# Performance work log

Measured on AMD Instinct MI355X. Metric: run time of the kernel, lower is better.

Reference implementation:

```python
import jax, jax.numpy as jnp
import numpy as np
from jax import lax

D_MODEL = 1024
D_STATE = 128
D_CONV = 4
EXPAND = 2
N_HEADS = 32
CHUNK = 64
D_INNER = EXPAND * D_MODEL                 # 2048
CONV_DIM = D_INNER + 2 * D_STATE           # 2304
D_IN_PROJ = 2 * D_INNER + 2 * D_STATE + N_HEADS  # 4384
HEAD_DIM = D_INNER // N_HEADS              # 64
EPS = 1e-5


def setup_inputs() -> dict:
    key = jax.random.key(0)
    ks = jax.random.split(key, 10)
    u = jax.random.normal(ks[0], (4, 4096, D_MODEL), dtype=jnp.float32)
    in_proj_w = jax.random.normal(ks[1], (D_IN_PROJ, D_MODEL), dtype=jnp.float32) * 0.02
    conv_w = jax.random.normal(ks[2], (CONV_DIM, 1, D_CONV), dtype=jnp.float32) * 0.3
    conv_b = jnp.zeros((CONV_DIM,), dtype=jnp.float32)
    dt_bias = jax.random.uniform(ks[3], (N_HEADS,), minval=-0.5, maxval=0.5, dtype=jnp.float32)
    A_log = jax.random.uniform(ks[4], (N_HEADS,), minval=-0.1, maxval=-0.01, dtype=jnp.float32)
    D = jax.random.uniform(ks[5], (N_HEADS,), minval=0.9, maxval=1.1, dtype=jnp.float32)
    norm_w = jnp.ones((D_INNER,), dtype=jnp.float32)
    out_proj_w = jax.random.normal(ks[6], (D_MODEL, D_INNER), dtype=jnp.float32) * 0.02
    return {"u": u, "in_proj_w": in_proj_w, "conv_w": conv_w, "conv_b": conv_b,
            "dt_bias": dt_bias, "A_log": A_log, "D": D, "norm_w": norm_w,
            "out_proj_w": out_proj_w}


def segsum(x):
    """Stable segment sum. x: (..., T) -> (..., T, T); exp of it is 1-semiseparable."""
    T = x.shape[-1]
    xe = jnp.broadcast_to(x[..., :, None], x.shape + (T,))  # '... d -> ... d e'
    mask_strict = jnp.tril(jnp.ones((T, T), dtype=bool), k=-1)
    xe = jnp.where(mask_strict, xe, 0.0)
    seg = jnp.cumsum(xe, axis=-2)
    mask_incl = jnp.tril(jnp.ones((T, T), dtype=bool), k=0)
    return jnp.where(mask_incl, seg, -jnp.inf)


def ssd(x, A, B, C):
    """x:(b,L,h,p)  A:(b,L,h)  B,C:(b,L,h,n). L multiple of CHUNK."""
    b, Lp, h, p = x.shape
    n = B.shape[-1]
    c = Lp // CHUNK
    x = x.reshape(b, c, CHUNK, h, p)
    A = A.reshape(b, c, CHUNK, h).transpose(0, 3, 1, 2)       # (b,h,c,l)
    B = B.reshape(b, c, CHUNK, h, n)
    C = C.reshape(b, c, CHUNK, h, n)
    A_cumsum = jnp.cumsum(A, axis=-1)                          # (b,h,c,l)
    L = jnp.exp(segsum(A))                                     # (b,h,c,l,l)
    # intra-chunk (diagonal blocks)
    Y_diag = jnp.einsum('bclhn,bcshn,bhcls,bcshp->bclhp', C, B, L, x)
    # chunk-final states
    decay_states = jnp.exp(A_cumsum[:, :, :, -1:] - A_cumsum)  # (b,h,c,l)
    states = jnp.einsum('bclhn,bhcl,bclhp->bchpn', B, decay_states, x)
    init = jnp.zeros_like(states[:, :1])
    states = jnp.concatenate([init, states], axis=1)           # (b,c+1,h,p,n)
    decay_chunk = jnp.exp(segsum(jnp.pad(A_cumsum[:, :, :, -1], ((0, 0), (0, 0), (1, 0)))))
    new_states = jnp.einsum('bhzc,bchpn->bzhpn', decay_chunk, states)
    states, final_state = new_states[:, :-1], new_states[:, -1]
    # inter-chunk (off-diagonal) contribution
    state_decay_out = jnp.exp(A_cumsum)
    Y_off = jnp.einsum('bclhn,bchpn,bhcl->bclhp', C, states, state_decay_out)
    Y = (Y_diag + Y_off).reshape(b, Lp, h, p)
    return Y, final_state


def _forward(u, in_proj_w, conv_w, conv_b, dt_bias, A_log, D, norm_w, out_proj_w):
    b, seq_len, _ = u.shape
    pad = CHUNK - seq_len % CHUNK  # note: full extra chunk when seq_len % CHUNK == 0 (faithful)
    u = jnp.pad(u, ((0, 0), (0, pad), (0, 0)))
    Lp = u.shape[1]
    A = -jnp.exp(A_log)                                        # (h,)
    zxbcdt = jnp.einsum('bld,ed->ble', u, in_proj_w)           # (b,Lp,D_IN_PROJ)
    z = zxbcdt[..., :D_INNER]
    xBC = zxbcdt[..., D_INNER:D_INNER + CONV_DIM]
    dt = zxbcdt[..., -N_HEADS:]
    # causal depthwise conv1d + silu
    xc = xBC.transpose(0, 2, 1)                                # (b,conv_dim,Lp)
    xc = lax.conv_general_dilated(xc, conv_w, window_strides=(1,),
                                  padding=[(D_CONV - 1, 0)],
                                  feature_group_count=CONV_DIM,
                                  dimension_numbers=('NCH', 'OIH', 'NCH'))
    xBC = jax.nn.silu((xc + conv_b[None, :, None]).transpose(0, 2, 1))
    x = xBC[..., :D_INNER].reshape(b, Lp, N_HEADS, HEAD_DIM)
    Bm = xBC[..., D_INNER:D_INNER + D_STATE]
    Cm = xBC[..., D_INNER + D_STATE:]
    Bm = jnp.broadcast_to(Bm[:, :, None, :], (b, Lp, N_HEADS, D_STATE))
    Cm = jnp.broadcast_to(Cm[:, :, None, :], (b, Lp, N_HEADS, D_STATE))
    dt = jax.nn.softplus(dt + dt_bias)                         # (b,Lp,h)
    y, _ = ssd(x * dt[..., None], A * dt, Bm, Cm)
    y = y + x * D[None, None, :, None]
    y = y.reshape(b, Lp, D_INNER)
    # gated RMSNorm
    t = y * jax.nn.silu(z)
    t = t * jax.lax.rsqrt(jnp.mean(t * t, axis=-1, keepdims=True) + EPS) * norm_w
    out = jnp.einsum('bld,ed->ble', t, out_proj_w)
    return out[:, :seq_len]


def reference(u, in_proj_w, conv_w, conv_b, dt_bias, A_log, D, norm_w, out_proj_w):
    return _forward(u, in_proj_w, conv_w, conv_b, dt_bias, A_log, D, norm_w, out_proj_w)
```

## Files before the change

### kernel.cpp

```cpp
#include <hip/hip_runtime.h>
#include <hip/hip_bf16.h>
#include <math.h>


#define BL    16384
#define NCONV 2304
#define LDXP  2336
#define STATE_ELEMS 16777216ull

typedef __hip_bfloat16 bf16;
typedef __attribute__((ext_vector_type(8))) short bf16x8_i;
typedef __attribute__((ext_vector_type(4))) float f32x4;

union BF8 { uint4 u; bf16 h[8]; };
union BF2 { uint u; bf16 h[2]; };

__device__ __forceinline__ void gload_lds16(const void* g, void* l) {
  __builtin_amdgcn_global_load_lds(
      (__attribute__((address_space(1))) void*)(uintptr_t)g,
      (__attribute__((address_space(3))) void*)(uint32_t)(uintptr_t)l,
      16, 0, 0);
}

template<typename TC, bool CLAMPB>
__global__ __launch_bounds__(256) void gemm_bt_mfma(
    const bf16* __restrict__ A, int lda,
    const bf16* __restrict__ B, int ldb,
    TC* __restrict__ C, int ldc, int N, int K)
{
  __shared__ __align__(16) bf16 As2[2][128 * 64];
  __shared__ __align__(16) bf16 Bs2[2][128 * 64];
  const int tid  = threadIdx.x;
  const int lane = tid & 63;
  const int wid  = tid >> 6;

  const int gx  = gridDim.x;
  const int nwg = gx * gridDim.y;
  const int q   = nwg >> 3;
  int id = blockIdx.y * gx + blockIdx.x;
  id = (id & 7) * q + (id >> 3);
  const int bm = (id / gx) * 128;
  const int bn = (id % gx) * 128;

  const int wr = (wid >> 1) * 64;
  const int wc = (wid & 1) * 64;

  f32x4 acc[4][4] = {};

  int aoff[4][2], boff[4][2];
  #pragma unroll
  for (int i = 0; i < 4; ++i) {
    const int ar = wr + i * 16 + (lane & 15);
    const int br = wc + i * 16 + (lane & 15);
    const int asw = ((ar >> 1) & 7) << 3;
    const int bsw = ((br >> 1) & 7) << 3;
    #pragma unroll
    for (int ks = 0; ks < 2; ++ks) {
      const int c0 = ks * 32 + (lane >> 4) * 8;
      aoff[i][ks] = ar * 64 + (c0 ^ asw);
      boff[i][ks] = br * 64 + (c0 ^ bsw);
    }
  }

  const int srow = tid >> 3;
  const int sj   = tid & 7;
  const bf16* pA[4];
  const bf16* pB[4];
  #pragma unroll
  for (int i = 0; i < 4; ++i) {
    const int r  = i * 32 + srow;
    const int js = sj ^ ((r >> 1) & 7);
    int brow = bn + r;
    if (CLAMPB) brow = min(brow, N - 1);
    pA[i] = A + (size_t)(bm + r) * lda + js * 8;
    pB[i] = B + (size_t)brow * ldb + js * 8;
  }

  const int NT = K >> 6;
  #pragma unroll
  for (int i = 0; i < 4; ++i) {
    gload_lds16(pA[i], &As2[0][0] + i * 2048 + wid * 512);
    gload_lds16(pB[i], &Bs2[0][0] + i * 2048 + wid * 512);
    pA[i] += 64; pB[i] += 64;
  }

  for (int t = 0; t < NT; ++t) {
    const int cur = t & 1;
    if (t + 1 < NT) {
      bf16* dA = &As2[cur ^ 1][0];
      bf16* dB = &Bs2[cur ^ 1][0];
      #pragma unroll
      for (int i = 0; i < 4; ++i) {
        gload_lds16(pA[i], dA + i * 2048 + wid * 512);
        gload_lds16(pB[i], dB + i * 2048 + wid * 512);
        pA[i] += 64; pB[i] += 64;
      }
      asm volatile("s_waitcnt vmcnt(8)" ::: "memory");
    } else {
      asm volatile("s_waitcnt vmcnt(0)" ::: "memory");
    }
    __builtin_amdgcn_sched_barrier(0);
    __builtin_amdgcn_s_barrier();
    const bf16* Ab = &As2[cur][0];
    const bf16* Bb = &Bs2[cur][0];
    __builtin_amdgcn_s_setprio(1);
    #pragma unroll
    for (int ks = 0; ks < 2; ++ks) {
      bf16x8_i af[4], bfr[4];
      #pragma unroll
      for (int i = 0; i < 4; ++i) {
        af[i]  = *(const bf16x8_i*)(Ab + aoff[i][ks]);
        bfr[i] = *(const bf16x8_i*)(Bb + boff[i][ks]);
      }
      #pragma unroll
      for (int i = 0; i < 4; ++i)
        #pragma unroll
        for (int j = 0; j < 4; ++j)
          acc[i][j] = __builtin_amdgcn_mfma_f32_16x16x32_bf16(
              af[i], bfr[j], acc[i][j], 0, 0, 0);
    }
    __builtin_amdgcn_s_setprio(0);
    __builtin_amdgcn_s_barrier();
  }

  const int cr = (lane >> 4) * 4;
  const int cc = lane & 15;
  #pragma unroll
  for (int i = 0; i < 4; ++i) {
    #pragma unroll
    for (int j = 0; j < 4; ++j) {
      const int n = bn + wc + j * 16 + cc;
      if (n < N) {
        #pragma unroll
        for (int r = 0; r < 4; ++r) {
          const int m = bm + wr + i * 16 + cr + r;
          if constexpr (sizeof(TC) == 2)
            ((bf16*)C)[(size_t)m * ldc + n] = __float2bfloat16(acc[i][j][r]);
          else
            ((float*)C)[(size_t)m * ldc + n] = acc[i][j][r];
        }
      }
    }
  }
}

__global__ __launch_bounds__(256) void cvt_f32_bf16(
    const float* __restrict__ in, bf16* __restrict__ out)
{
  const size_t i = (size_t)(blockIdx.x * 256 + threadIdx.x) * 8;
  float4 a = *(const float4*)(in + i);
  float4 b = *(const float4*)(in + i + 4);
  BF8 o;
  o.h[0] = __float2bfloat16(a.x); o.h[1] = __float2bfloat16(a.y);
  o.h[2] = __float2bfloat16(a.z); o.h[3] = __float2bfloat16(a.w);
  o.h[4] = __float2bfloat16(b.x); o.h[5] = __float2bfloat16(b.y);
  o.h[6] = __float2bfloat16(b.z); o.h[7] = __float2bfloat16(b.w);
  *(uint4*)(out + i) = o.u;
}

__global__ __launch_bounds__(256) void dtsp_atot_kernel(
    const bf16* __restrict__ xpre, const float* __restrict__ dt_bias,
    const float* __restrict__ A_log,
    float* __restrict__ dtT, float* __restrict__ Atot)
{
  const int c = blockIdx.x, b = blockIdx.y;
  const int tid = threadIdx.x;
  const int h = tid & 31, lg = tid >> 5;
  __shared__ float red[8][33];
  float s = 0.f, vals[8];
  const bf16* src = xpre + ((size_t)b * 4096 + c * 64 + lg * 8) * LDXP + 2304 + h;
  const float bias = dt_bias[h];
  #pragma unroll
  for (int k = 0; k < 8; ++k) {
    float v = __bfloat162float(src[(size_t)k * LDXP]) + bias;
    v = fmaxf(v, 0.f) + log1pf(expf(-fabsf(v)));
    vals[k] = v; s += v;
  }
  float* dp = dtT + ((size_t)(b * 32 + h)) * 4096 + c * 64 + lg * 8;
  #pragma unroll
  for (int k = 0; k < 8; ++k) dp[k] = vals[k];
  red[lg][h] = s;
  __syncthreads();
  if (tid < 32) {
    float t = 0.f;
    #pragma unroll
    for (int g = 0; g < 8; ++g) t += red[g][tid];
    Atot[((size_t)b * 64 + c) * 32 + tid] = -expf(A_log[tid]) * t;
  }
}

__global__ __launch_bounds__(256) void conv_silu_kernel(
    const bf16* __restrict__ xpre,
    const float* __restrict__ conv_w,
    const float* __restrict__ conv_b,
    bf16* __restrict__ xBC)
{
  const int ch = blockIdx.x * 256 + threadIdx.x;
  const int t0 = blockIdx.y * 8;
  const int bb = blockIdx.z;
  const float w0 = conv_w[ch*4+0], w1 = conv_w[ch*4+1];
  const float w2 = conv_w[ch*4+2], w3 = conv_w[ch*4+3];
  const float bias = conv_b[ch];
  const size_t rb = (size_t)bb * 4096;
  const bf16* src = xpre + ch;
  float v0 = (t0 >= 3) ? __bfloat162float(src[(rb + t0 - 3) * LDXP]) : 0.f;
  float v1 = (t0 >= 2) ? __bfloat162float(src[(rb + t0 - 2) * LDXP]) : 0.f;
  float v2 = (t0 >= 1) ? __bfloat162float(src[(rb + t0 - 1) * LDXP]) : 0.f;
  for (int t = t0; t < t0 + 8; ++t) {
    float v3 = __bfloat162float(src[(rb + t) * LDXP]);
    float o = bias + w0*v0 + w1*v1 + w2*v2 + w3*v3;
    o = o / (1.f + expf(-o));
    xBC[(rb + t) * NCONV + ch] = __float2bfloat16(o);
    v0 = v1; v1 = v2; v2 = v3;
  }
}

__device__ __forceinline__ int swz8(int row) { return ((row >> 3) & 7) << 3; }

__global__ __launch_bounds__(256) void s0_scores(
    const bf16* __restrict__ xBC, float* __restrict__ sc_raw)
{
  const int c = blockIdx.x, b = blockIdx.y;
  const int tid = threadIdx.x, lane = tid & 63, wid = tid >> 6;
  __shared__ bf16 Bc[64 * 136];
  __shared__ bf16 Cc[64 * 136];
  const size_t r0 = (size_t)b * 4096 + (size_t)c * 64;
  #pragma unroll
  for (int k = 0; k < 4; ++k) {
    int id = tid + k * 256, l = id >> 4, n0 = (id & 15) * 8;
    *(uint4*)(Bc + l * 136 + n0) =
        *(const uint4*)(xBC + (r0 + l) * NCONV + 2048 + n0);
    *(uint4*)(Cc + l * 136 + n0) =
        *(const uint4*)(xBC + (r0 + l) * NCONV + 2176 + n0);
  }
  __syncthreads();
  const int wr  = (wid & 1) * 32;
  const int wcs = (wid >> 1) * 32;
  f32x4 as[2][2] = {};
  #pragma unroll
  for (int ks = 0; ks < 4; ++ks) {
    const int k0 = ks * 32 + (lane >> 4) * 8;
    bf16x8_i af[2], bfr[2];
    #pragma unroll
    for (int i = 0; i < 2; ++i)
      af[i] = *(const bf16x8_i*)(Cc + (wr + i * 16 + (lane & 15)) * 136 + k0);
    #pragma unroll
    for (int j = 0; j < 2; ++j)
      bfr[j] = *(const bf16x8_i*)(Bc + (wcs + j * 16 + (lane & 15)) * 136 + k0);
    #pragma unroll
    for (int i = 0; i < 2; ++i)
      #pragma unroll
      for (int j = 0; j < 2; ++j)
        as[i][j] = __builtin_amdgcn_mfma_f32_16x16x32_bf16(
            af[i], bfr[j], as[i][j], 0, 0, 0);
  }
  float* dst = sc_raw + ((size_t)(b * 64 + c)) * 4096;
  const int cr = (lane >> 4) * 4, cc = lane & 15;
  #pragma unroll
  for (int i = 0; i < 2; ++i)
    #pragma unroll
    for (int r = 0; r < 4; ++r) {
      const int l = wr + i * 16 + cr + r;
      #pragma unroll
      for (int j = 0; j < 2; ++j)
        dst[l * 64 + wcs + j * 16 + cc] = as[i][j][r];
    }
}

__global__ __launch_bounds__(256) void s1_localstate(
    const bf16* __restrict__ xBC, const float* __restrict__ dtT,
    const float* __restrict__ A_log, bf16* __restrict__ states, int bbase)
{
  const int hh = blockIdx.x, c = blockIdx.y;
  const int b  = bbase + blockIdx.z;
  const int tid = threadIdx.x, lane = tid & 63, wid = tid >> 6;
  __shared__ bf16 BT[128 * 72];
  __shared__ bf16 xwT[64 * 72];
  __shared__ bf16 Sout[64 * 136];
  const size_t r0 = (size_t)b * 4096 + (size_t)c * 64;

  BF8 regB[4], regx[2];
  #pragma unroll
  for (int k = 0; k < 4; ++k) {
    int id = tid + k * 256, l = id >> 4, n0 = (id & 15) * 8;
    regB[k].u = *(const uint4*)(xBC + (r0 + l) * NCONV + 2048 + n0);
  }
  #pragma unroll
  for (int k = 0; k < 2; ++k) {
    int id = tid + k * 256, l = id >> 3, p0 = (id & 7) * 8;
    regx[k].u = *(const uint4*)(xBC + (r0 + l) * NCONV + hh * 64 + p0);
  }

  float d = dtT[((size_t)(b * 32 + hh)) * 4096 + c * 64 + lane];
  float Ah = -expf(A_log[hh]);
  float v = Ah * d;
  #pragma unroll
  for (int off = 1; off < 64; off <<= 1) {
    float up = __shfl_up(v, off, 64);
    if (lane >= off) v += up;
  }
  const float At = __shfl(v, 63, 64);
  const float w = d * __expf(At - v);

  #pragma unroll
  for (int k = 0; k < 4; ++k) {
    int id = tid + k * 256, l = id >> 4, n0 = (id & 15) * 8;
    #pragma unroll
    for (int j = 0; j < 8; ++j) {
      int n = n0 + j;
      BT[n * 72 + (l ^ swz8(n))] = regB[k].h[j];
    }
  }
  #pragma unroll
  for (int k = 0; k < 2; ++k) {
    int id = tid + k * 256, l = id >> 3, p0 = (id & 7) * 8;
    float wv = __shfl(w, l, 64);
    #pragma unroll
    for (int j = 0; j < 8; ++j) {
      int p = p0 + j;
      xwT[p * 72 + (l ^ swz8(p))] =
          __float2bfloat16(__bfloat162float(regx[k].h[j]) * wv);
    }
  }
  __syncthreads();

  const int wr = (wid & 1) * 32;
  const int wc = (wid >> 1) * 64;
  f32x4 acc[2][4] = {};
  #pragma unroll
  for (int ks = 0; ks < 2; ++ks) {
    const int k0 = ks * 32 + (lane >> 4) * 8;
    bf16x8_i a[2], bb[4];
    #pragma unroll
    for (int i = 0; i < 2; ++i) {
      int p = wr + i * 16 + (lane & 15);
      a[i] = *(const bf16x8_i*)(xwT + p * 72 + (k0 ^ swz8(p)));
    }
    #pragma unroll
    for (int j = 0; j < 4; ++j) {
      int n = wc + j * 16 + (lane & 15);
      bb[j] = *(const bf16x8_i*)(BT + n * 72 + (k0 ^ swz8(n)));
    }
    #pragma unroll
    for (int i = 0; i < 2; ++i)
      #pragma unroll
      for (int j = 0; j < 4; ++j)
        acc[i][j] = __builtin_amdgcn_mfma_f32_16x16x32_bf16(
            a[i], bb[j], acc[i][j], 0, 0, 0);
  }

  const int cr = (lane >> 4) * 4, cn = lane & 15;
  #pragma unroll
  for (int i = 0; i < 2; ++i)
    #pragma unroll
    for (int j = 0; j < 4; ++j)
      #pragma unroll
      for (int r = 0; r < 4; ++r)
        Sout[(wr + i * 16 + cr + r) * 136 + (wc + j * 16 + cn)] =
            __float2bfloat16(acc[i][j][r]);
  __syncthreads();
  bf16* sb = states + (size_t)blockIdx.z * STATE_ELEMS
                    + ((size_t)c * 32 + hh) * 8192;
  #pragma unroll
  for (int k = 0; k < 4; ++k) {
    int id = tid + k * 256, p = id >> 4, n0 = (id & 15) * 8;
    *(uint4*)(sb + p * 128 + n0) = *(const uint4*)(Sout + p * 136 + n0);
  }
}

#define S2STEP(R, CI)                                                     \
  {                                                                       \
    BF2 o;                                                                \
    o.h[0] = __float2bfloat16(ca); o.h[1] = __float2bfloat16(cb);         \
    const float e = ec[CI];                                               \
    ca = fmaf(e, ca, __bfloat162float(R.h[0]));                           \
    cb = fmaf(e, cb, __bfloat162float(R.h[1]));                           \
    *(uint*)(ptr + (size_t)(CI) * cs) = o.u;                              \
    if ((CI) + 8 < 64) R.u = *(const uint*)(ptr + (size_t)((CI) + 8) * cs); \
  }

__global__ __launch_bounds__(256) void s2_scan(
    bf16* __restrict__ states, const float* __restrict__ Atot, int bbase)
{
  const int h  = blockIdx.x >> 4;
  const int p  = ((blockIdx.x & 15) << 2) | (threadIdx.x >> 6);
  const int n0 = (threadIdx.x & 63) * 2;
  const int b  = bbase + blockIdx.y;
  __shared__ float ec[64];
  if (threadIdx.x < 64)
    ec[threadIdx.x] = expf(Atot[((size_t)b * 64 + threadIdx.x) * 32 + h]);
  __syncthreads();
  bf16* ptr = states + (size_t)blockIdx.y * STATE_ELEMS
                     + ((size_t)h * 64 + p) * 128 + n0;
  const size_t cs = (size_t)32 * 8192;
  float ca = 0.f, cb = 0.f;
  BF2 r0, r1, r2, r3, r4, r5, r6, r7;
  r0.u = *(const uint*)(ptr + 0 * cs);
  r1.u = *(const uint*)(ptr + 1 * cs);
  r2.u = *(const uint*)(ptr + 2 * cs);
  r3.u = *(const uint*)(ptr + 3 * cs);
  r4.u = *(const uint*)(ptr + 4 * cs);
  r5.u = *(const uint*)(ptr + 5 * cs);
  r6.u = *(const uint*)(ptr + 6 * cs);
  r7.u = *(const uint*)(ptr + 7 * cs);
  for (int g = 0; g < 8; ++g) {
    const int c0 = g * 8;
    S2STEP(r0, c0 + 0); S2STEP(r1, c0 + 1);
    S2STEP(r2, c0 + 2); S2STEP(r3, c0 + 3);
    S2STEP(r4, c0 + 4); S2STEP(r5, c0 + 5);
    S2STEP(r6, c0 + 6); S2STEP(r7, c0 + 7);
  }
}

__global__ __launch_bounds__(256) void s3_output(
    const bf16* __restrict__ xBC, const float* __restrict__ dtT,
    const float* __restrict__ A_log, const float* __restrict__ Dp,
    const bf16* __restrict__ states, const float* __restrict__ sc_raw,
    bf16* __restrict__ Y, int bbase)
{
  const int hh = blockIdx.x, c = blockIdx.y;
  const int b  = bbase + blockIdx.z;
  const int tid = threadIdx.x, lane = tid & 63, wid = tid >> 6;
  __shared__ bf16 Cc[64 * 136];
  __shared__ bf16 Yb[64 * 136];
  __shared__ bf16 Sin[64 * 136];
  __shared__ bf16 xT[64 * 72];
  __shared__ bf16 scb[64 * 72];
  __shared__ float Ac[64], dts[64];
  const size_t r0 = (size_t)b * 4096 + (size_t)c * 64;

  if (tid < 64) {
    float d = dtT[((size_t)(b * 32 + hh)) * 4096 + c * 64 + tid];
    float Ah = -expf(A_log[hh]);
    float v = Ah * d;
    #pragma unroll
    for (int off = 1; off < 64; off <<= 1) {
      float up = __shfl_up(v, off, 64);
      if (tid >= off) v += up;
    }
    Ac[tid] = v; dts[tid] = d;
  }

  #pragma unroll
  for (int k = 0; k < 4; ++k) {
    int id = tid + k * 256, l = id >> 4, n0 = (id & 15) * 8;
    *(uint4*)(Cc + l * 136 + n0) =
        *(const uint4*)(xBC + (r0 + l) * NCONV + 2176 + n0);
  }
  const bf16* sb = states + (size_t)blockIdx.z * STATE_ELEMS
                          + ((size_t)c * 32 + hh) * 8192;
  #pragma unroll
  for (int k = 0; k < 4; ++k) {
    int id = tid + k * 256, p = id >> 4, n0 = (id & 15) * 8;
    *(uint4*)(Sin + p * 136 + n0) = *(const uint4*)(sb + p * 128 + n0);
  }
  #pragma unroll
  for (int k = 0; k < 2; ++k) {
    int id = tid + k * 256, l = id >> 3, p0 = (id & 7) * 8;
    BF8 v; v.u = *(const uint4*)(xBC + (r0 + l) * NCONV + hh * 64 + p0);
    #pragma unroll
    for (int j = 0; j < 8; ++j) {
      int p = p0 + j;
      xT[p * 72 + (l ^ swz8(p))] = v.h[j];
    }
  }
  __syncthreads();

  const int wr  = (wid & 1) * 32;
  const int wcs = (wid >> 1) * 32;
  bf16x8_i afrag[2][4];
  #pragma unroll
  for (int ks = 0; ks < 4; ++ks) {
    const int k0 = ks * 32 + (lane >> 4) * 8;
    #pragma unroll
    for (int i = 0; i < 2; ++i)
      afrag[i][ks] =
          *(const bf16x8_i*)(Cc + (wr + i * 16 + (lane & 15)) * 136 + k0);
  }
  {
    const float* scr = sc_raw + ((size_t)(b * 64 + c)) * 4096;
    #pragma unroll
    for (int k = 0; k < 4; ++k) {
      int idx = tid + k * 256;
      int l = idx >> 4, s0 = (idx & 15) * 4;
      float4 v = *(const float4*)(scr + l * 64 + s0);
      const float acl = Ac[l];
      float vv[4] = {v.x, v.y, v.z, v.w};
      #pragma unroll
      for (int j = 0; j < 4; ++j) {
        int s = s0 + j;
        float val = (s <= l) ? vv[j] * __expf(acl - Ac[s]) * dts[s] : 0.f;
        scb[l * 72 + s] = __float2bfloat16(val);
      }
    }
  }
  __syncthreads();

  f32x4 ay[2][2] = {};
  #pragma unroll
  for (int ks = 0; ks < 4; ++ks) {
    const int k0 = ks * 32 + (lane >> 4) * 8;
    #pragma unroll
    for (int j = 0; j < 2; ++j) {
      bf16x8_i bfr =
          *(const bf16x8_i*)(Sin + (wcs + j * 16 + (lane & 15)) * 136 + k0);
      #pragma unroll
      for (int i = 0; i < 2; ++i)
        ay[i][j] = __builtin_amdgcn_mfma_f32_16x16x32_bf16(
            afrag[i][ks], bfr, ay[i][j], 0, 0, 0);
    }
  }
  const int cr = (lane >> 4) * 4, cc = lane & 15;
  #pragma unroll
  for (int i = 0; i < 2; ++i)
    #pragma unroll
    for (int r = 0; r < 4; ++r) {
      const float dk = __expf(Ac[wr + i * 16 + cr + r]);
      #pragma unroll
      for (int j = 0; j < 2; ++j) ay[i][j][r] *= dk;
    }
  #pragma unroll
  for (int ks = 0; ks < 2; ++ks) {
    const int k0 = ks * 32 + (lane >> 4) * 8;
    bf16x8_i a2[2], b2[2];
    #pragma unroll
    for (int i = 0; i < 2; ++i)
      a2[i] = *(const bf16x8_i*)(scb + (wr + i * 16 + (lane & 15)) * 72 + k0);
    #pragma unroll
    for (int j = 0; j < 2; ++j) {
      int p = wcs + j * 16 + (lane & 15);
      b2[j] = *(const bf16x8_i*)(xT + p * 72 + (k0 ^ swz8(p)));
    }
    #pragma unroll
    for (int i = 0; i < 2; ++i)
      #pragma unroll
      for (int j = 0; j < 2; ++j)
        ay[i][j] = __builtin_amdgcn_mfma_f32_16x16x32_bf16(
            a2[i], b2[j], ay[i][j], 0, 0, 0);
  }
  const float Dh = Dp[hh];
  #pragma unroll
  for (int i = 0; i < 2; ++i)
    #pragma unroll
    for (int r = 0; r < 4; ++r) {
      const int l = wr + i * 16 + cr + r;
      #pragma unroll
      for (int j = 0; j < 2; ++j) {
        const int p = wcs + j * 16 + cc;
        float xv = __bfloat162float(xT[p * 72 + (l ^ swz8(p))]);
        Yb[l * 136 + p] = __float2bfloat16(ay[i][j][r] + Dh * xv);
      }
    }
  __syncthreads();
  #pragma unroll
  for (int k = 0; k < 2; ++k) {
    int id = tid + k * 256, l = id >> 3, p0 = (id & 7) * 8;
    *(uint4*)(Y + (r0 + l) * 2048 + hh * 64 + p0) =
        *(const uint4*)(Yb + l * 136 + p0);
  }
}

__global__ __launch_bounds__(256) void gate_rmsnorm_kernel(
    bf16* __restrict__ y, const bf16* __restrict__ z,
    const float* __restrict__ norm_w)
{
  const size_t row = blockIdx.x;
  const int tid = threadIdx.x;
  __shared__ float red[4];
  const bf16* zr = z + row * 2048;
  bf16* yr = y + row * 2048;
  BF8 zv, yv;
  zv.u = *(const uint4*)(zr + tid * 8);
  yv.u = *(const uint4*)(yr + tid * 8);
  float t[8];
  float local = 0.f;
  #pragma unroll
  for (int j = 0; j < 8; ++j) {
    float zz = __bfloat162float(zv.h[j]);
    float yy = __bfloat162float(yv.h[j]);
    float tv = yy * (zz / (1.f + expf(-zz)));
    t[j] = tv;
    local += tv * tv;
  }
  #pragma unroll
  for (int off = 32; off; off >>= 1) local += __shfl_down(local, off, 64);
  if ((tid & 63) == 0) red[tid >> 6] = local;
  __syncthreads();
  const float total = red[0] + red[1] + red[2] + red[3];
  const float scale = rsqrtf(total * (1.f / 2048.f) + 1e-5f);
  BF8 o;
  #pragma unroll
  for (int j = 0; j < 8; ++j)
    o.h[j] = __float2bfloat16(t[j] * scale * norm_w[tid * 8 + j]);
  *(uint4*)(yr + tid * 8) = o.u;
}

extern "C" void kernel_launch(void* const* d_in, const int* in_sizes, int n_in,
                              void* d_out, int out_size, void* d_ws, size_t ws_size,
                              hipStream_t stream) {
  (void)in_sizes; (void)n_in; (void)out_size;
  const float* u          = (const float*)d_in[0];
  const float* in_proj_w  = (const float*)d_in[1];
  const float* conv_w     = (const float*)d_in[2];
  const float* conv_b     = (const float*)d_in[3];
  const float* dt_bias    = (const float*)d_in[4];
  const float* A_log      = (const float*)d_in[5];
  const float* Dp         = (const float*)d_in[6];
  const float* norm_w     = (const float*)d_in[7];
  const float* out_proj_w = (const float*)d_in[8];
  float* out = (float*)d_out;

  char* ws = (char*)d_ws;
  bf16*  u_bf   = (bf16*)ws;
  bf16*  xpre   = (bf16*)(ws + 33554432);
  bf16*  xBCc   = (bf16*)(ws + 110100480);
  float* dtT    = (float*)(ws + 185597952);
  bf16*  W_all  = (bf16*)(ws + 187695104);
  bf16*  W_z    = W_all;
  bf16*  W_xpre = W_all + (size_t)2048 * 1024;
  bf16*  out_w  = (bf16*)(ws + 196673536);
  float* Atot   = (float*)(ws + 200867840);
  bf16*  states = (bf16*)(ws + 200900608);
  bf16*  ybuf   = xpre;
  bf16*  zbuf   = xBCc;
  float* sc_raw = (float*)(ws + 100663296);

  const int NB = (ws_size >= 268009472ull) ? 2 : 1;

  cvt_f32_bf16<<<dim3(8192), 256, 0, stream>>>(u, u_bf);
  cvt_f32_bf16<<<dim3(2192), 256, 0, stream>>>(in_proj_w, W_all);
  cvt_f32_bf16<<<dim3(1024), 256, 0, stream>>>(out_proj_w, out_w);
  gemm_bt_mfma<bf16, true><<<dim3(19, 128), 256, 0, stream>>>(
      u_bf, 1024, W_xpre, 1024, xpre, LDXP, 2336, 1024);
  dtsp_atot_kernel<<<dim3(64, 4), 256, 0, stream>>>(xpre, dt_bias, A_log,
                                                    dtT, Atot);
  conv_silu_kernel<<<dim3(9, 512, 4), 256, 0, stream>>>(xpre, conv_w, conv_b,
                                                        xBCc);
  s0_scores<<<dim3(64, 4), 256, 0, stream>>>(xBCc, sc_raw);
  for (int b0 = 0; b0 < 4; b0 += NB) {
    s1_localstate<<<dim3(32, 64, NB), 256, 0, stream>>>(xBCc, dtT, A_log,
                                                        states, b0);
    s2_scan<<<dim3(512, NB), 256, 0, stream>>>(states, Atot, b0);
    s3_output<<<dim3(32, 64, NB), 256, 0, stream>>>(xBCc, dtT, A_log, Dp,
                                                    states, sc_raw, ybuf, b0);
  }
  gemm_bt_mfma<bf16, false><<<dim3(16, 128), 256, 0, stream>>>(
      u_bf, 1024, W_z, 1024, zbuf, 2048, 2048, 1024);
  gate_rmsnorm_kernel<<<dim3(BL), 256, 0, stream>>>(ybuf, zbuf, norm_w);
  gemm_bt_mfma<float, false><<<dim3(8, 128), 256, 0, stream>>>(
      ybuf, 2048, out_w, 2048, out, 1024, 1024, 2048);
}
```

Before: 503.5 us.

## Enlarge GEMM tiles to 256x256 with 8 waves per workgroup

Reworks the bf16 MFMA GEMM from 128x128 tiles with 4 waves to 256x256 tiles with 8 waves (512 threads), each wave computing a 128x64 sub-tile with 8x4 accumulators. The goal is more operand reuse per LDS load and fewer global loads per FLOP across all three projection GEMMs. In exchange, LDS use doubles to 128KB per block, register pressure rises, and the grids shrink to 640, 512 and 256 workgroups, which could limit occupancy and fill across CUs. The xpre GEMM now pads N to 2560 against 2336, wasting more clamped work.

New measurement: 530.5 us. 1.05x slower.

```diff
diff --git a/kernel.cpp b/kernel.cpp
--- a/kernel.cpp
+++ b/kernel.cpp
@@ -23,53 +23,48 @@
 }
 
 template<typename TC, bool CLAMPB>
-__global__ __launch_bounds__(256) void gemm_bt_mfma(
+__global__ __launch_bounds__(512) void gemm_bt_mfma(
     const bf16* __restrict__ A, int lda,
     const bf16* __restrict__ B, int ldb,
     TC* __restrict__ C, int ldc, int N, int K)
 {
-  __shared__ __align__(16) bf16 As2[2][128 * 64];
-  __shared__ __align__(16) bf16 Bs2[2][128 * 64];
+  __shared__ __align__(16) bf16 As2[2][16384];
+  __shared__ __align__(16) bf16 Bs2[2][16384];
   const int tid  = threadIdx.x;
   const int lane = tid & 63;
   const int wid  = tid >> 6;
+  const int wm   = wid >> 2;
+  const int wn   = wid & 3;
 
   const int gx  = gridDim.x;
   const int nwg = gx * gridDim.y;
   const int q   = nwg >> 3;
   int id = blockIdx.y * gx + blockIdx.x;
   id = (id & 7) * q + (id >> 3);
-  const int bm = (id / gx) * 128;
-  const int bn = (id % gx) * 128;
-
-  const int wr = (wid >> 1) * 64;
-  const int wc = (wid & 1) * 64;
-
-  f32x4 acc[4][4] = {};
-
-  int aoff[4][2], boff[4][2];
-  #pragma unroll
-  for (int i = 0; i < 4; ++i) {
-    const int ar = wr + i * 16 + (lane & 15);
-    const int br = wc + i * 16 + (lane & 15);
-    const int asw = ((ar >> 1) & 7) << 3;
-    const int bsw = ((br >> 1) & 7) << 3;
-    #pragma unroll
-    for (int ks = 0; ks < 2; ++ks) {
-      const int c0 = ks * 32 + (lane >> 4) * 8;
-      aoff[i][ks] = ar * 64 + (c0 ^ asw);
-      boff[i][ks] = br * 64 + (c0 ^ bsw);
-    }
+  const int bm = (id / gx) * 256;
+  const int bn = (id % gx) * 256;
+
+  f32x4 acc[8][4] = {};
+
+  int aoff[8], boff[4];
+  #pragma unroll
+  for (int mf = 0; mf < 8; ++mf) {
+    const int ar = wm * 128 + mf * 16 + (lane & 15);
+    aoff[mf] = ar * 64 + (((lane >> 4) * 8) ^ (((ar >> 1) & 7) << 3));
+  }
+  #pragma unroll
+  for (int nf = 0; nf < 4; ++nf) {
+    const int br = wn * 64 + nf * 16 + (lane & 15);
+    boff[nf] = br * 64 + (((lane >> 4) * 8) ^ (((br >> 1) & 7) << 3));
   }
 
   const int srow = tid >> 3;
-  const int sj   = tid & 7;
+  const int js   = (tid & 7) ^ ((srow >> 1) & 7);
   const bf16* pA[4];
   const bf16* pB[4];
   #pragma unroll
   for (int i = 0; i < 4; ++i) {
-    const int r  = i * 32 + srow;
-    const int js = sj ^ ((r >> 1) & 7);
+    const int r = i * 64 + srow;
     int brow = bn + r;
     if (CLAMPB) brow = min(brow, N - 1);
     pA[i] = A + (size_t)(bm + r) * lda + js * 8;
@@ -79,8 +74,8 @@
   const int NT = K >> 6;
   #pragma unroll
   for (int i = 0; i < 4; ++i) {
-    gload_lds16(pA[i], &As2[0][0] + i * 2048 + wid * 512);
-    gload_lds16(pB[i], &Bs2[0][0] + i * 2048 + wid * 512);
+    gload_lds16(pA[i], &As2[0][0] + i * 4096 + wid * 512);
+    gload_lds16(pB[i], &Bs2[0][0] + i * 4096 + wid * 512);
     pA[i] += 64; pB[i] += 64;
   }
 
@@ -91,8 +86,8 @@
       bf16* dB = &Bs2[cur ^ 1][0];
       #pragma unroll
       for (int i = 0; i < 4; ++i) {
-        gload_lds16(pA[i], dA + i * 2048 + wid * 512);
-        gload_lds16(pB[i], dB + i * 2048 + wid * 512);
+        gload_lds16(pA[i], dA + i * 4096 + wid * 512);
+        gload_lds16(pB[i], dB + i * 4096 + wid * 512);
         pA[i] += 64; pB[i] += 64;
       }
       asm volatile("s_waitcnt vmcnt(8)" ::: "memory");
@@ -106,18 +101,20 @@
     __builtin_amdgcn_s_setprio(1);
     #pragma unroll
     for (int ks = 0; ks < 2; ++ks) {
-      bf16x8_i af[4], bfr[4];
-      #pragma unroll
-      for (int i = 0; i < 4; ++i) {
-        af[i]  = *(const bf16x8_i*)(Ab + aoff[i][ks]);
-        bfr[i] = *(const bf16x8_i*)(Bb + boff[i][ks]);
-      }
-      #pragma unroll
-      for (int i = 0; i < 4; ++i)
+      const int kx = ks * 32;
+      bf16x8_i bfr[4], af[8];
+      #pragma unroll
+      for (int nf = 0; nf < 4; ++nf)
+        bfr[nf] = *(const bf16x8_i*)(Bb + (boff[nf] ^ kx));
+      #pragma unroll
+      for (int mf = 0; mf < 8; ++mf)
+        af[mf] = *(const bf16x8_i*)(Ab + (aoff[mf] ^ kx));
+      #pragma unroll
+      for (int mf = 0; mf < 8; ++mf)
         #pragma unroll
-        for (int j = 0; j < 4; ++j)
-          acc[i][j] = __builtin_amdgcn_mfma_f32_16x16x32_bf16(
-              af[i], bfr[j], acc[i][j], 0, 0, 0);
+        for (int nf = 0; nf < 4; ++nf)
+          acc[mf][nf] = __builtin_amdgcn_mfma_f32_16x16x32_bf16(
+              af[mf], bfr[nf], acc[mf][nf], 0, 0, 0);
     }
     __builtin_amdgcn_s_setprio(0);
     __builtin_amdgcn_s_barrier();
@@ -126,18 +123,18 @@
   const int cr = (lane >> 4) * 4;
   const int cc = lane & 15;
   #pragma unroll
-  for (int i = 0; i < 4; ++i) {
-    #pragma unroll
-    for (int j = 0; j < 4; ++j) {
-      const int n = bn + wc + j * 16 + cc;
+  for (int mf = 0; mf < 8; ++mf) {
+    #pragma unroll
+    for (int nf = 0; nf < 4; ++nf) {
+      const int n = bn + wn * 64 + nf * 16 + cc;
       if (n < N) {
         #pragma unroll
         for (int r = 0; r < 4; ++r) {
-          const int m = bm + wr + i * 16 + cr + r;
+          const int m = bm + wm * 128 + mf * 16 + cr + r;
           if constexpr (sizeof(TC) == 2)
-            ((bf16*)C)[(size_t)m * ldc + n] = __float2bfloat16(acc[i][j][r]);
+            ((bf16*)C)[(size_t)m * ldc + n] = __float2bfloat16(acc[mf][nf][r]);
           else
-            ((float*)C)[(size_t)m * ldc + n] = acc[i][j][r];
+            ((float*)C)[(size_t)m * ldc + n] = acc[mf][nf][r];
         }
       }
     }
@@ -630,7 +627,7 @@
   cvt_f32_bf16<<<dim3(8192), 256, 0, stream>>>(u, u_bf);
   cvt_f32_bf16<<<dim3(2192), 256, 0, stream>>>(in_proj_w, W_all);
   cvt_f32_bf16<<<dim3(1024), 256, 0, stream>>>(out_proj_w, out_w);
-  gemm_bt_mfma<bf16, true><<<dim3(19, 128), 256, 0, stream>>>(
+  gemm_bt_mfma<bf16, true><<<dim3(10, 64), 512, 0, stream>>>(
       u_bf, 1024, W_xpre, 1024, xpre, LDXP, 2336, 1024);
   dtsp_atot_kernel<<<dim3(64, 4), 256, 0, stream>>>(xpre, dt_bias, A_log,
                                                     dtT, Atot);
@@ -644,9 +641,9 @@
     s3_output<<<dim3(32, 64, NB), 256, 0, stream>>>(xBCc, dtT, A_log, Dp,
                                                     states, sc_raw, ybuf, b0);
   }
-  gemm_bt_mfma<bf16, false><<<dim3(16, 128), 256, 0, stream>>>(
+  gemm_bt_mfma<bf16, false><<<dim3(8, 64), 512, 0, stream>>>(
       u_bf, 1024, W_z, 1024, zbuf, 2048, 2048, 1024);
   gate_rmsnorm_kernel<<<dim3(BL), 256, 0, stream>>>(ybuf, zbuf, norm_w);
-  gemm_bt_mfma<float, false><<<dim3(8, 128), 256, 0, stream>>>(
+  gemm_bt_mfma<float, false><<<dim3(4, 64), 512, 0, stream>>>(
       ybuf, 2048, out_w, 2048, out, 1024, 1024, 2048);
 }
```

## Fuse gating and RMSNorm into z-projection and out-projection GEMM epilogues

Applied to the files above, without the earlier changes.

The z GEMM epilogue now reads y, applies the silu(z) gate in place, and writes per-64-column partial sums of squares. A small kernel turns these into per-row rsqrt scales. The out-projection GEMM applies that row scale in its epilogue, and norm_w is folded into the bf16 weight conversion. This removes the separate gate_rmsnorm pass and the write and read of the z buffer, at the cost of strided bf16 read-modify-write in the GEMM epilogue and applying the row scale after the matmul rather than before.

New measurement: 519.9 us. +3.3%, slower.

```diff
diff --git a/kernel.cpp b/kernel.cpp
--- a/kernel.cpp
+++ b/kernel.cpp
@@ -22,11 +22,12 @@
       16, 0, 0);
 }
 
-template<typename TC, bool CLAMPB>
+template<typename TC, bool CLAMPB, int MODE>
 __global__ __launch_bounds__(256) void gemm_bt_mfma(
     const bf16* __restrict__ A, int lda,
     const bf16* __restrict__ B, int ldb,
-    TC* __restrict__ C, int ldc, int N, int K)
+    TC* __restrict__ C, int ldc, int N, int K,
+    float* __restrict__ partial, const float* __restrict__ rowscale)
 {
   __shared__ __align__(16) bf16 As2[2][128 * 64];
   __shared__ __align__(16) bf16 Bs2[2][128 * 64];
@@ -125,22 +126,74 @@
 
   const int cr = (lane >> 4) * 4;
   const int cc = lane & 15;
-  #pragma unroll
-  for (int i = 0; i < 4; ++i) {
-    #pragma unroll
-    for (int j = 0; j < 4; ++j) {
-      const int n = bn + wc + j * 16 + cc;
-      if (n < N) {
+  if constexpr (MODE == 0) {
+    #pragma unroll
+    for (int i = 0; i < 4; ++i) {
+      #pragma unroll
+      for (int j = 0; j < 4; ++j) {
+        const int n = bn + wc + j * 16 + cc;
+        if (n < N) {
+          #pragma unroll
+          for (int r = 0; r < 4; ++r) {
+            const int m = bm + wr + i * 16 + cr + r;
+            if constexpr (sizeof(TC) == 2)
+              ((bf16*)C)[(size_t)m * ldc + n] = __float2bfloat16(acc[i][j][r]);
+            else
+              ((float*)C)[(size_t)m * ldc + n] = acc[i][j][r];
+          }
+        }
+      }
+    }
+  } else if constexpr (MODE == 1) {
+    float s_[4][4] = {{0.f,0.f,0.f,0.f},{0.f,0.f,0.f,0.f},
+                      {0.f,0.f,0.f,0.f},{0.f,0.f,0.f,0.f}};
+    #pragma unroll
+    for (int i = 0; i < 4; ++i)
+      #pragma unroll
+      for (int j = 0; j < 4; ++j) {
+        const int n = bn + wc + j * 16 + cc;
         #pragma unroll
         for (int r = 0; r < 4; ++r) {
           const int m = bm + wr + i * 16 + cr + r;
-          if constexpr (sizeof(TC) == 2)
-            ((bf16*)C)[(size_t)m * ldc + n] = __float2bfloat16(acc[i][j][r]);
-          else
-            ((float*)C)[(size_t)m * ldc + n] = acc[i][j][r];
+          const float z = acc[i][j][r];
+          const float y = __bfloat162float(((const bf16*)C)[(size_t)m * ldc + n]);
+          const float g = y * (z / (1.f + __expf(-z)));
+          ((bf16*)C)[(size_t)m * ldc + n] = __float2bfloat16(g);
+          s_[i][r] += g * g;
         }
       }
-    }
+    #pragma unroll
+    for (int i = 0; i < 4; ++i)
+      #pragma unroll
+      for (int r = 0; r < 4; ++r) {
+        float v = s_[i][r];
+        v += __shfl_xor(v, 1, 64);
+        v += __shfl_xor(v, 2, 64);
+        v += __shfl_xor(v, 4, 64);
+        v += __shfl_xor(v, 8, 64);
+        s_[i][r] = v;
+      }
+    if ((lane & 15) == 0) {
+      const int ccq = (bn + wc) >> 6;
+      #pragma unroll
+      for (int i = 0; i < 4; ++i)
+        #pragma unroll
+        for (int r = 0; r < 4; ++r)
+          partial[(size_t)ccq * BL + (bm + wr + i * 16 + cr + r)] = s_[i][r];
+    }
+  } else {
+    #pragma unroll
+    for (int i = 0; i < 4; ++i)
+      #pragma unroll
+      for (int r = 0; r < 4; ++r) {
+        const int m = bm + wr + i * 16 + cr + r;
+        const float sc = rowscale[m];
+        #pragma unroll
+        for (int j = 0; j < 4; ++j) {
+          const int n = bn + wc + j * 16 + cc;
+          ((float*)C)[(size_t)m * ldc + n] = acc[i][j][r] * sc;
+        }
+      }
   }
 }
 
@@ -156,6 +209,34 @@
   o.h[4] = __float2bfloat16(b.x); o.h[5] = __float2bfloat16(b.y);
   o.h[6] = __float2bfloat16(b.z); o.h[7] = __float2bfloat16(b.w);
   *(uint4*)(out + i) = o.u;
+}
+
+__global__ __launch_bounds__(256) void cvt_wout_norm(
+    const float* __restrict__ w, const float* __restrict__ norm_w,
+    bf16* __restrict__ out)
+{
+  const size_t i = (size_t)(blockIdx.x * 256 + threadIdx.x) * 8;
+  const int k0 = (int)(i & 2047);
+  float4 a = *(const float4*)(w + i);
+  float4 b = *(const float4*)(w + i + 4);
+  float4 na = *(const float4*)(norm_w + k0);
+  float4 nb = *(const float4*)(norm_w + k0 + 4);
+  BF8 o;
+  o.h[0] = __float2bfloat16(a.x * na.x); o.h[1] = __float2bfloat16(a.y * na.y);
+  o.h[2] = __float2bfloat16(a.z * na.z); o.h[3] = __float2bfloat16(a.w * na.w);
+  o.h[4] = __float2bfloat16(b.x * nb.x); o.h[5] = __float2bfloat16(b.y * nb.y);
+  o.h[6] = __float2bfloat16(b.z * nb.z); o.h[7] = __float2bfloat16(b.w * nb.w);
+  *(uint4*)(out + i) = o.u;
+}
+
+__global__ __launch_bounds__(256) void finalize_scale(
+    const float* __restrict__ partial, float* __restrict__ rowscale)
+{
+  const int m = blockIdx.x * 256 + threadIdx.x;
+  float s = 0.f;
+  #pragma unroll
+  for (int q = 0; q < 32; ++q) s += partial[(size_t)q * BL + m];
+  rowscale[m] = rsqrtf(s * (1.f / 2048.f) + 1e-5f);
 }
 
 __global__ __launch_bounds__(256) void dtsp_atot_kernel(
@@ -560,41 +641,6 @@
   }
 }
 
-__global__ __launch_bounds__(256) void gate_rmsnorm_kernel(
-    bf16* __restrict__ y, const bf16* __restrict__ z,
-    const float* __restrict__ norm_w)
-{
-  const size_t row = blockIdx.x;
-  const int tid = threadIdx.x;
-  __shared__ float red[4];
-  const bf16* zr = z + row * 2048;
-  bf16* yr = y + row * 2048;
-  BF8 zv, yv;
-  zv.u = *(const uint4*)(zr + tid * 8);
-  yv.u = *(const uint4*)(yr + tid * 8);
-  float t[8];
-  float local = 0.f;
-  #pragma unroll
-  for (int j = 0; j < 8; ++j) {
-    float zz = __bfloat162float(zv.h[j]);
-    float yy = __bfloat162float(yv.h[j]);
-    float tv = yy * (zz / (1.f + expf(-zz)));
-    t[j] = tv;
-    local += tv * tv;
-  }
-  #pragma unroll
-  for (int off = 32; off; off >>= 1) local += __shfl_down(local, off, 64);
-  if ((tid & 63) == 0) red[tid >> 6] = local;
-  __syncthreads();
-  const float total = red[0] + red[1] + red[2] + red[3];
-  const float scale = rsqrtf(total * (1.f / 2048.f) + 1e-5f);
-  BF8 o;
-  #pragma unroll
-  for (int j = 0; j < 8; ++j)
-    o.h[j] = __float2bfloat16(t[j] * scale * norm_w[tid * 8 + j]);
-  *(uint4*)(yr + tid * 8) = o.u;
-}
-
 extern "C" void kernel_launch(void* const* d_in, const int* in_sizes, int n_in,
                               void* d_out, int out_size, void* d_ws, size_t ws_size,
                               hipStream_t stream) {
@@ -622,16 +668,17 @@
   float* Atot   = (float*)(ws + 200867840);
   bf16*  states = (bf16*)(ws + 200900608);
   bf16*  ybuf   = xpre;
-  bf16*  zbuf   = xBCc;
   float* sc_raw = (float*)(ws + 100663296);
+  float* partial  = (float*)xBCc;
+  float* rowscale = partial + (size_t)32 * BL;
 
   const int NB = (ws_size >= 268009472ull) ? 2 : 1;
 
   cvt_f32_bf16<<<dim3(8192), 256, 0, stream>>>(u, u_bf);
   cvt_f32_bf16<<<dim3(2192), 256, 0, stream>>>(in_proj_w, W_all);
-  cvt_f32_bf16<<<dim3(1024), 256, 0, stream>>>(out_proj_w, out_w);
-  gemm_bt_mfma<bf16, true><<<dim3(19, 128), 256, 0, stream>>>(
-      u_bf, 1024, W_xpre, 1024, xpre, LDXP, 2336, 1024);
+  cvt_wout_norm<<<dim3(1024), 256, 0, stream>>>(out_proj_w, norm_w, out_w);
+  gemm_bt_mfma<bf16, true, 0><<<dim3(19, 128), 256, 0, stream>>>(
+      u_bf, 1024, W_xpre, 1024, xpre, LDXP, 2336, 1024, nullptr, nullptr);
   dtsp_atot_kernel<<<dim3(64, 4), 256, 0, stream>>>(xpre, dt_bias, A_log,
                                                     dtT, Atot);
   conv_silu_kernel<<<dim3(9, 512, 4), 256, 0, stream>>>(xpre, conv_w, conv_b,
@@ -644,9 +691,9 @@
     s3_output<<<dim3(32, 64, NB), 256, 0, stream>>>(xBCc, dtT, A_log, Dp,
                                                     states, sc_raw, ybuf, b0);
   }
-  gemm_bt_mfma<bf16, false><<<dim3(16, 128), 256, 0, stream>>>(
-      u_bf, 1024, W_z, 1024, zbuf, 2048, 2048, 1024);
-  gate_rmsnorm_kernel<<<dim3(BL), 256, 0, stream>>>(ybuf, zbuf, norm_w);
-  gemm_bt_mfma<float, false><<<dim3(8, 128), 256, 0, stream>>>(
-      ybuf, 2048, out_w, 2048, out, 1024, 1024, 2048);
-}
+  gemm_bt_mfma<bf16, false, 1><<<dim3(16, 128), 256, 0, stream>>>(
+      u_bf, 1024, W_z, 1024, ybuf, 2048, 2048, 1024, partial, nullptr);
+  finalize_scale<<<dim3(64), 256, 0, stream>>>(partial, rowscale);
+  gemm_bt_mfma<float, false, 2><<<dim3(8, 128), 256, 0, stream>>>(
+      ybuf, 2048, out_w, 2048, out, 1024, 1024, 2048, nullptr, rowscale);
+}
```
